# Kernel tuning notes

Hardware: AMD Instinct MI355X
Metric: run time of the kernel (lower is better)

Reference implementation:

```python
import jax, jax.numpy as jnp
import numpy as np

V = 100000
E = 1250000
C_IN = 64
C_OUT = 64


def setup_inputs() -> dict:
    key = jax.random.key(0)
    ks = jax.random.split(key, 6)
    X = jax.random.normal(ks[0], (V, C_IN), dtype=jnp.float32)
    edge_src = jax.random.randint(ks[1], (E,), 0, V, dtype=jnp.int32)
    edge_dst = jax.random.randint(ks[2], (E,), 0, V, dtype=jnp.int32)
    edge_w = jax.random.uniform(ks[3], (E,), dtype=jnp.float32)
    # xavier_normal for (C_IN, C_OUT) weight
    std = float(np.sqrt(2.0 / (C_IN + C_OUT)))
    W = jax.random.normal(ks[4], (C_IN, C_OUT), dtype=jnp.float32) * std
    b = jax.random.normal(ks[5], (C_OUT,), dtype=jnp.float32) * 0.0  # bias init zeros
    return {"X": X, "edge_src": edge_src, "edge_dst": edge_dst,
            "edge_w": edge_w, "W": W, "b": b}


def reference(X, edge_src, edge_dst, edge_w, W, b):
    # f = A @ X  (sparse COO spmm): f[dst] += w * X[src]
    msgs = edge_w[:, None] * X[edge_src]                 # [E, C_IN]
    f = jax.ops.segment_sum(msgs, edge_dst, num_segments=X.shape[0])  # [V, C_IN]
    # out = f @ W + b
    return f @ W + b
```

## Files before the change

kernel.cpp:

```cpp
#include <hip/hip_runtime.h>
#include <hip/hip_fp16.h>


constexpr int V = 100000;
constexpr int E = 1250000;
constexpr int C = 64;

constexpr int NBKT = 1024;
constexpr int VB   = 98;
constexpr int BCAP = 1536;
constexpr int FL   = 8;
constexpr int OVF_CAP = 16384;

constexpr size_t Y_OFF    = 0;
constexpr size_t BIN_OFF  = 12800000;
constexpr size_t GCNT_OFF = 25382912;
constexpr size_t OC_OFF   = 25387008;
constexpr size_t OVF_OFF  = 25387024;
constexpr size_t WS_NEW   = 25649168;

using bf16x8 = __attribute__((ext_vector_type(8))) short;
using f32x4  = __attribute__((ext_vector_type(4))) float;

__device__ __forceinline__ short f2bf(float x) {
    unsigned u = __float_as_uint(x);
    unsigned r = u + 0x7fffu + ((u >> 16) & 1u);
    return (short)(r >> 16);
}
__device__ __forceinline__ float bf2f(short h) {
    return __uint_as_float(((unsigned)(unsigned short)h) << 16);
}

constexpr int ZB  = 1;
constexpr int NBM = 1563;

__global__ __launch_bounds__(256) void zero_xw_kernel(const float* __restrict__ X,
                                                      const float* __restrict__ W,
                                                      __half* __restrict__ Y,
                                                      int* __restrict__ gcnt,
                                                      int* __restrict__ oc) {
    if (blockIdx.x < ZB) {
        int i = threadIdx.x;
        #pragma unroll
        for (int j = 0; j < NBKT / 256; ++j) gcnt[i + j * 256] = 0;
        if (i == 0) *oc = 0;
        return;
    }
    __shared__ short Whi[64 * 72];
    __shared__ short Wlo[64 * 72];
    for (int idx = threadIdx.x; idx < 4096; idx += 256) {
        int k = idx >> 6, c = idx & 63;
        float w  = W[idx];
        short hi = f2bf(w);
        short lo = f2bf(w - bf2f(hi));
        Whi[c * 72 + k] = hi;
        Wlo[c * 72 + k] = lo;
    }
    __syncthreads();

    const int wave = threadIdx.x >> 6;
    const int lane = threadIdx.x & 63;
    const int m = lane & 15;
    const int q = lane >> 4;

    bf16x8 bhi[4][2], blo[4][2];
    #pragma unroll
    for (int t = 0; t < 4; ++t)
        #pragma unroll
        for (int h = 0; h < 2; ++h) {
            int o = (t * 16 + m) * 72 + h * 32 + q * 8;
            bhi[t][h] = *(const bf16x8*)&Whi[o];
            blo[t][h] = *(const bf16x8*)&Wlo[o];
        }

    const int chunk = (blockIdx.x - ZB) * 4 + wave;
    if (chunk >= V / 16) return;
    {
        const float* xp = X + (chunk * 16 + m) * 64 + q * 8;
        bf16x8 ahi[2], alo[2];
        #pragma unroll
        for (int h = 0; h < 2; ++h) {
            float4 f0 = *(const float4*)(xp + h * 32);
            float4 f1 = *(const float4*)(xp + h * 32 + 4);
            float f[8] = {f0.x, f0.y, f0.z, f0.w, f1.x, f1.y, f1.z, f1.w};
            #pragma unroll
            for (int j = 0; j < 8; ++j) {
                short hi = f2bf(f[j]);
                ahi[h][j] = hi;
                alo[h][j] = f2bf(f[j] - bf2f(hi));
            }
        }
        #pragma unroll
        for (int t = 0; t < 4; ++t) {
            f32x4 acc = {0.f, 0.f, 0.f, 0.f};
            #pragma unroll
            for (int h = 0; h < 2; ++h) {
                acc = __builtin_amdgcn_mfma_f32_16x16x32_bf16(ahi[h], bhi[t][h], acc, 0, 0, 0);
                acc = __builtin_amdgcn_mfma_f32_16x16x32_bf16(alo[h], bhi[t][h], acc, 0, 0, 0);
                acc = __builtin_amdgcn_mfma_f32_16x16x32_bf16(ahi[h], blo[t][h], acc, 0, 0, 0);
            }
            #pragma unroll
            for (int i = 0; i < 4; ++i) {
                int row = chunk * 16 + q * 4 + i;
                Y[row * 64 + t * 16 + m] = __float2half(acc[i]);
            }
        }
    }
}

constexpr int BIN_BLOCKS = 512;
constexpr int BIN_T      = 1024;

__global__ __launch_bounds__(BIN_T) void bin_kernel(const int*   __restrict__ esrc,
                                                    const int*   __restrict__ edst,
                                                    const float* __restrict__ ew,
                                                    int*  __restrict__ gcnt,
                                                    int2* __restrict__ binned,
                                                    int*  __restrict__ oc,
                                                    int4* __restrict__ ovf) {
    __shared__ int2 stage[NBKT][FL];
    __shared__ int  lcnt[NBKT];
    for (int i = threadIdx.x; i < NBKT; i += BIN_T) lcnt[i] = 0;
    __syncthreads();

    const int iters = (E + BIN_BLOCKS * BIN_T - 1) / (BIN_BLOCKS * BIN_T);
    for (int it = 0; it < iters; ++it) {
        int e = (it * BIN_BLOCKS + blockIdx.x) * BIN_T + threadIdx.x;
        if (e < E) {
            int d = edst[e];
            int s = esrc[e];
            float w = ew[e];
            int bkt = d / VB;
            int ld  = d - bkt * VB;
            int2 rec = make_int2((ld << 17) | s, __float_as_int(w));
            int pos = atomicAdd(&lcnt[bkt], 1);
            if (pos < FL) {
                stage[bkt][pos] = rec;
            } else {
                int g = atomicAdd(&gcnt[bkt], 1);
                if (g < BCAP) binned[bkt * BCAP + g] = rec;
                else { int p = atomicAdd(oc, 1);
                       if (p < OVF_CAP) ovf[p] = make_int4(s, d, __float_as_int(w), 0); }
            }
        }
    }
    __syncthreads();
    for (int b = threadIdx.x; b < NBKT; b += BIN_T) {
        int n = lcnt[b]; n = n < FL ? n : FL;
        if (n > 0) {
            int g = atomicAdd(&gcnt[b], n);
            for (int i = 0; i < n; ++i) {
                int gi = g + i;
                int2 r = stage[b][i];
                if (gi < BCAP) binned[b * BCAP + gi] = r;
                else { int s = r.x & 0x1FFFF; int ld = r.x >> 17;
                       int p = atomicAdd(oc, 1);
                       if (p < OVF_CAP) ovf[p] = make_int4(s, b * VB + ld, r.y, 0); }
            }
        }
    }
}

__global__ __launch_bounds__(512) void bucket_gather_kernel(const int*  __restrict__ gcnt,
                                                            const int2* __restrict__ binned,
                                                            const int*  __restrict__ oc,
                                                            const int4* __restrict__ ovf,
                                                            const __half* __restrict__ Y,
                                                            const float* __restrict__ bias,
                                                            float* __restrict__ out) {
    __shared__ int2 raw[BCAP];
    __shared__ int2 sorted[BCAP];
    __shared__ int  cnt[VB];
    __shared__ int  pre[VB];
    __shared__ int  cur[VB];
    __shared__ int  buf[128];

    const int tid = threadIdx.x;
    const int b   = blockIdx.x;
    int n = gcnt[b]; n = n < BCAP ? n : BCAP;

    for (int i = tid; i < VB; i += 512) cnt[i] = 0;
    __syncthreads();

    const int2* src = binned + b * BCAP;
    for (int i = tid; i < n; i += 512) {
        int2 r = src[i];
        raw[i] = r;
        atomicAdd(&cnt[r.x >> 17], 1);
    }
    __syncthreads();

    int x = 0;
    if (tid < 128) { x = (tid < VB) ? cnt[tid] : 0; buf[tid] = x; }
    __syncthreads();
    #pragma unroll
    for (int ofs = 1; ofs < 128; ofs <<= 1) {
        int t = 0;
        if (tid < 128 && tid >= ofs) t = buf[tid - ofs];
        __syncthreads();
        if (tid < 128) buf[tid] += t;
        __syncthreads();
    }
    if (tid < VB) { int ex = buf[tid] - x; pre[tid] = ex; cur[tid] = ex; }
    __syncthreads();

    for (int i = tid; i < n; i += 512) {
        int2 r = raw[i];
        int ld = r.x >> 17;
        int p = atomicAdd(&cur[ld], 1);
        sorted[p] = r;
    }
    __syncthreads();

    const int lane = tid & 63;
    const int wv   = tid >> 6;
    float bias_l = bias[lane];
    int ovn = *oc; ovn = ovn < OVF_CAP ? ovn : OVF_CAP;

    for (int ld = wv; ld < VB; ld += 8) {
        int v = b * VB + ld;
        if (v >= V) break;
        int beg = pre[ld];
        int end = beg + cnt[ld];
        float acc = 0.f;
        int i = beg;
        for (; i + 8 <= end; i += 8) {
            int2 r0 = sorted[i],     r1 = sorted[i + 1];
            int2 r2 = sorted[i + 2], r3 = sorted[i + 3];
            int2 r4 = sorted[i + 4], r5 = sorted[i + 5];
            int2 r6 = sorted[i + 6], r7 = sorted[i + 7];
            float y0 = __half2float(Y[(r0.x & 0x1FFFF) * C + lane]);
            float y1 = __half2float(Y[(r1.x & 0x1FFFF) * C + lane]);
            float y2 = __half2float(Y[(r2.x & 0x1FFFF) * C + lane]);
            float y3 = __half2float(Y[(r3.x & 0x1FFFF) * C + lane]);
            float y4 = __half2float(Y[(r4.x & 0x1FFFF) * C + lane]);
            float y5 = __half2float(Y[(r5.x & 0x1FFFF) * C + lane]);
            float y6 = __half2float(Y[(r6.x & 0x1FFFF) * C + lane]);
            float y7 = __half2float(Y[(r7.x & 0x1FFFF) * C + lane]);
            acc += __int_as_float(r0.y) * y0;
            acc += __int_as_float(r1.y) * y1;
            acc += __int_as_float(r2.y) * y2;
            acc += __int_as_float(r3.y) * y3;
            acc += __int_as_float(r4.y) * y4;
            acc += __int_as_float(r5.y) * y5;
            acc += __int_as_float(r6.y) * y6;
            acc += __int_as_float(r7.y) * y7;
        }
        for (; i + 4 <= end; i += 4) {
            int2 r0 = sorted[i], r1 = sorted[i + 1], r2 = sorted[i + 2], r3 = sorted[i + 3];
            float y0 = __half2float(Y[(r0.x & 0x1FFFF) * C + lane]);
            float y1 = __half2float(Y[(r1.x & 0x1FFFF) * C + lane]);
            float y2 = __half2float(Y[(r2.x & 0x1FFFF) * C + lane]);
            float y3 = __half2float(Y[(r3.x & 0x1FFFF) * C + lane]);
            acc += __int_as_float(r0.y) * y0;
            acc += __int_as_float(r1.y) * y1;
            acc += __int_as_float(r2.y) * y2;
            acc += __int_as_float(r3.y) * y3;
        }
        for (; i < end; ++i) {
            int2 rr = sorted[i];
            acc += __int_as_float(rr.y) * __half2float(Y[(rr.x & 0x1FFFF) * C + lane]);
        }
        for (int k = 0; k < ovn; ++k) {
            int4 rr = ovf[k];
            if (rr.y == v)
                acc += __int_as_float(rr.z) * __half2float(Y[rr.x * C + lane]);
        }
        out[v * C + lane] = acc + bias_l;
    }
}

__global__ __launch_bounds__(256) void xw_kernel(const float* __restrict__ X,
                                                 const float* __restrict__ W,
                                                 float* __restrict__ Y) {
    __shared__ float Ws[64][64];
    const float4* W4 = (const float4*)W;
    float4* Ws4 = (float4*)&Ws[0][0];
    #pragma unroll
    for (int i = 0; i < 4; ++i)
        Ws4[threadIdx.x + 256 * i] = W4[threadIdx.x + 256 * i];
    __syncthreads();
    const int wave = threadIdx.x >> 6;
    const int lane = threadIdx.x & 63;
    for (int row = blockIdx.x * 4 + wave; row < V; row += gridDim.x * 4) {
        float xv = X[row * C + lane];
        float acc = 0.f;
        #pragma unroll
        for (int k = 0; k < C; ++k)
            acc += __shfl(xv, k, 64) * Ws[k][lane];
        Y[row * C + lane] = acc;
    }
}

__global__ __launch_bounds__(256) void init_out_kernel(const float* __restrict__ b,
                                                       float4* __restrict__ out4) {
    int tid = blockIdx.x * 256 + threadIdx.x;
    const int n4 = V * (C / 4);
    if (tid < n4) {
        const float4* b4 = (const float4*)b;
        out4[tid] = b4[tid & 15];
    }
}

__global__ __launch_bounds__(256) void scatter_kernel(const int*   __restrict__ esrc,
                                                      const int*   __restrict__ edst,
                                                      const float* __restrict__ ew,
                                                      const float* __restrict__ Y,
                                                      float*       __restrict__ out) {
    unsigned tid = blockIdx.x * 256u + threadIdx.x;
    unsigned e = tid >> 4;
    if (e >= (unsigned)E) return;
    int g = (tid & 15) * 4;
    int   s  = esrc[e];
    int   d  = edst[e];
    float we = ew[e];
    float4 y = *(const float4*)(Y + s * C + g);
    float* o = out + (size_t)d * C + g;
    atomicAdd(o + 0, we * y.x);
    atomicAdd(o + 1, we * y.y);
    atomicAdd(o + 2, we * y.z);
    atomicAdd(o + 3, we * y.w);
}

extern "C" void kernel_launch(void* const* d_in, const int* in_sizes, int n_in,
                              void* d_out, int out_size, void* d_ws, size_t ws_size,
                              hipStream_t stream) {
    const float* X    = (const float*)d_in[0];
    const int*   esrc = (const int*)  d_in[1];
    const int*   edst = (const int*)  d_in[2];
    const float* ew   = (const float*)d_in[3];
    const float* W    = (const float*)d_in[4];
    const float* b    = (const float*)d_in[5];
    float* out = (float*)d_out;

    char* ws = (char*)d_ws;

    if (ws_size >= WS_NEW) {
        __half* Y     = (__half*)(ws + Y_OFF);
        int2*  binned = (int2*)(ws + BIN_OFF);
        int*   gcnt   = (int*) (ws + GCNT_OFF);
        int*   oc     = (int*) (ws + OC_OFF);
        int4*  ovf    = (int4*)(ws + OVF_OFF);

        zero_xw_kernel<<<ZB + NBM, 256, 0, stream>>>(X, W, Y, gcnt, oc);
        bin_kernel<<<BIN_BLOCKS, BIN_T, 0, stream>>>(esrc, edst, ew, gcnt, binned, oc, ovf);
        bucket_gather_kernel<<<NBKT, 512, 0, stream>>>(gcnt, binned, oc, ovf, Y, b, out);
    } else {
        float* Y = (float*)(ws + Y_OFF);
        xw_kernel<<<1024, 256, 0, stream>>>(X, W, Y);
        init_out_kernel<<<(V * (C / 4) + 255) / 256, 256, 0, stream>>>(b, (float4*)out);
        scatter_kernel<<<(E * 16 + 255) / 256, 256, 0, stream>>>(esrc, edst, ew, Y, out);
    }
}
```

Measured before the change: 142.7 us.

## Fuse X·W transform and edge binning into one interleaved kernel launch

Merges the dense X·W MFMA kernel and the edge-binning kernel into a single launch. Blocks are interleaved three XW blocks to two bin blocks, and shared memory is a union of the two stages' buffers. The zeroing of bucket counters moves to a tiny separate kernel. The aim is to overlap the compute-bound GEMM with the atomic-heavy binning and to drop a launch boundary, at the cost of 512-thread bin blocks (down from 1024), more loop iterations, and an extra launch for zeroing.

```diff
diff --git a/kernel.cpp b/kernel.cpp
--- a/kernel.cpp
+++ b/kernel.cpp
@@ -31,131 +31,141 @@
     return __uint_as_float(((unsigned)(unsigned short)h) << 16);
 }
 
-constexpr int ZB  = 1;
-constexpr int NBM = 1563;
-
-__global__ __launch_bounds__(256) void zero_xw_kernel(const float* __restrict__ X,
-                                                      const float* __restrict__ W,
-                                                      __half* __restrict__ Y,
-                                                      int* __restrict__ gcnt,
-                                                      int* __restrict__ oc) {
-    if (blockIdx.x < ZB) {
-        int i = threadIdx.x;
+__global__ __launch_bounds__(256) void zero_kernel(int* __restrict__ gcnt,
+                                                   int* __restrict__ oc) {
+    int i = threadIdx.x;
+    #pragma unroll
+    for (int j = 0; j < NBKT / 256; ++j) gcnt[i + j * 256] = 0;
+    if (i == 0) *oc = 0;
+}
+
+constexpr int FUSE_T    = 512;
+constexpr int XWB       = 782;
+constexpr int BINB      = 512;
+constexpr int FUSE_GRID = 261 * 5;
+
+__global__ __launch_bounds__(FUSE_T) void xwbin_kernel(
+        const float* __restrict__ X,
+        const float* __restrict__ W,
+        __half*      __restrict__ Y,
+        const int*   __restrict__ esrc,
+        const int*   __restrict__ edst,
+        const float* __restrict__ ew,
+        int*  __restrict__ gcnt,
+        int2* __restrict__ binned,
+        int*  __restrict__ oc,
+        int4* __restrict__ ovf) {
+    __shared__ union {
+        struct { short Whi[64 * 72]; short Wlo[64 * 72]; } xw;
+        struct { int2 stage[NBKT][FL]; int lcnt[NBKT]; } bin;
+    } u;
+
+    const int grp  = blockIdx.x / 5;
+    const int slot = blockIdx.x % 5;
+
+    if (slot < 3) {
+        const int xb = grp * 3 + slot;
+        if (xb >= XWB) return;
+
+        for (int idx = threadIdx.x; idx < 4096; idx += FUSE_T) {
+            int k = idx >> 6, c = idx & 63;
+            float w  = W[idx];
+            short hi = f2bf(w);
+            short lo = f2bf(w - bf2f(hi));
+            u.xw.Whi[c * 72 + k] = hi;
+            u.xw.Wlo[c * 72 + k] = lo;
+        }
+        __syncthreads();
+
+        const int wave = threadIdx.x >> 6;
+        const int lane = threadIdx.x & 63;
+        const int m = lane & 15;
+        const int q = lane >> 4;
+
+        bf16x8 bhi[4][2], blo[4][2];
         #pragma unroll
-        for (int j = 0; j < NBKT / 256; ++j) gcnt[i + j * 256] = 0;
-        if (i == 0) *oc = 0;
-        return;
-    }
-    __shared__ short Whi[64 * 72];
-    __shared__ short Wlo[64 * 72];
-    for (int idx = threadIdx.x; idx < 4096; idx += 256) {
-        int k = idx >> 6, c = idx & 63;
-        float w  = W[idx];
-        short hi = f2bf(w);
-        short lo = f2bf(w - bf2f(hi));
-        Whi[c * 72 + k] = hi;
-        Wlo[c * 72 + k] = lo;
-    }
-    __syncthreads();
-
-    const int wave = threadIdx.x >> 6;
-    const int lane = threadIdx.x & 63;
-    const int m = lane & 15;
-    const int q = lane >> 4;
-
-    bf16x8 bhi[4][2], blo[4][2];
-    #pragma unroll
-    for (int t = 0; t < 4; ++t)
-        #pragma unroll
-        for (int h = 0; h < 2; ++h) {
-            int o = (t * 16 + m) * 72 + h * 32 + q * 8;
-            bhi[t][h] = *(const bf16x8*)&Whi[o];
-            blo[t][h] = *(const bf16x8*)&Wlo[o];
-        }
-
-    const int chunk = (blockIdx.x - ZB) * 4 + wave;
-    if (chunk >= V / 16) return;
-    {
-        const float* xp = X + (chunk * 16 + m) * 64 + q * 8;
-        bf16x8 ahi[2], alo[2];
-        #pragma unroll
-        for (int h = 0; h < 2; ++h) {
-            float4 f0 = *(const float4*)(xp + h * 32);
-            float4 f1 = *(const float4*)(xp + h * 32 + 4);
-            float f[8] = {f0.x, f0.y, f0.z, f0.w, f1.x, f1.y, f1.z, f1.w};
-            #pragma unroll
-            for (int j = 0; j < 8; ++j) {
-                short hi = f2bf(f[j]);
-                ahi[h][j] = hi;
-                alo[h][j] = f2bf(f[j] - bf2f(hi));
-            }
-        }
-        #pragma unroll
-        for (int t = 0; t < 4; ++t) {
-            f32x4 acc = {0.f, 0.f, 0.f, 0.f};
+        for (int t = 0; t < 4; ++t)
             #pragma unroll
             for (int h = 0; h < 2; ++h) {
-                acc = __builtin_amdgcn_mfma_f32_16x16x32_bf16(ahi[h], bhi[t][h], acc, 0, 0, 0);
-                acc = __builtin_amdgcn_mfma_f32_16x16x32_bf16(alo[h], bhi[t][h], acc, 0, 0, 0);
-                acc = __builtin_amdgcn_mfma_f32_16x16x32_bf16(ahi[h], blo[t][h], acc, 0, 0, 0);
-            }
+                int o = (t * 16 + m) * 72 + h * 32 + q * 8;
+                bhi[t][h] = *(const bf16x8*)&u.xw.Whi[o];
+                blo[t][h] = *(const bf16x8*)&u.xw.Wlo[o];
+            }
+
+        const int chunk = xb * 8 + wave;
+        if (chunk >= V / 16) return;
+        {
+            const float* xp = X + (chunk * 16 + m) * 64 + q * 8;
+            bf16x8 ahi[2], alo[2];
             #pragma unroll
-            for (int i = 0; i < 4; ++i) {
-                int row = chunk * 16 + q * 4 + i;
-                Y[row * 64 + t * 16 + m] = __float2half(acc[i]);
-            }
-        }
-    }
-}
-
-constexpr int BIN_BLOCKS = 512;
-constexpr int BIN_T      = 1024;
-
-__global__ __launch_bounds__(BIN_T) void bin_kernel(const int*   __restrict__ esrc,
-                                                    const int*   __restrict__ edst,
-                                                    const float* __restrict__ ew,
-                                                    int*  __restrict__ gcnt,
-                                                    int2* __restrict__ binned,
-                                                    int*  __restrict__ oc,
-                                                    int4* __restrict__ ovf) {
-    __shared__ int2 stage[NBKT][FL];
-    __shared__ int  lcnt[NBKT];
-    for (int i = threadIdx.x; i < NBKT; i += BIN_T) lcnt[i] = 0;
-    __syncthreads();
-
-    const int iters = (E + BIN_BLOCKS * BIN_T - 1) / (BIN_BLOCKS * BIN_T);
-    for (int it = 0; it < iters; ++it) {
-        int e = (it * BIN_BLOCKS + blockIdx.x) * BIN_T + threadIdx.x;
-        if (e < E) {
-            int d = edst[e];
-            int s = esrc[e];
-            float w = ew[e];
-            int bkt = d / VB;
-            int ld  = d - bkt * VB;
-            int2 rec = make_int2((ld << 17) | s, __float_as_int(w));
-            int pos = atomicAdd(&lcnt[bkt], 1);
-            if (pos < FL) {
-                stage[bkt][pos] = rec;
-            } else {
-                int g = atomicAdd(&gcnt[bkt], 1);
-                if (g < BCAP) binned[bkt * BCAP + g] = rec;
-                else { int p = atomicAdd(oc, 1);
-                       if (p < OVF_CAP) ovf[p] = make_int4(s, d, __float_as_int(w), 0); }
-            }
-        }
-    }
-    __syncthreads();
-    for (int b = threadIdx.x; b < NBKT; b += BIN_T) {
-        int n = lcnt[b]; n = n < FL ? n : FL;
-        if (n > 0) {
-            int g = atomicAdd(&gcnt[b], n);
-            for (int i = 0; i < n; ++i) {
-                int gi = g + i;
-                int2 r = stage[b][i];
-                if (gi < BCAP) binned[b * BCAP + gi] = r;
-                else { int s = r.x & 0x1FFFF; int ld = r.x >> 17;
-                       int p = atomicAdd(oc, 1);
-                       if (p < OVF_CAP) ovf[p] = make_int4(s, b * VB + ld, r.y, 0); }
+            for (int h = 0; h < 2; ++h) {
+                float4 f0 = *(const float4*)(xp + h * 32);
+                float4 f1 = *(const float4*)(xp + h * 32 + 4);
+                float f[8] = {f0.x, f0.y, f0.z, f0.w, f1.x, f1.y, f1.z, f1.w};
+                #pragma unroll
+                for (int j = 0; j < 8; ++j) {
+                    short hi = f2bf(f[j]);
+                    ahi[h][j] = hi;
+                    alo[h][j] = f2bf(f[j] - bf2f(hi));
+                }
+            }
+            #pragma unroll
+            for (int t = 0; t < 4; ++t) {
+                f32x4 acc = {0.f, 0.f, 0.f, 0.f};
+                #pragma unroll
+                for (int h = 0; h < 2; ++h) {
+                    acc = __builtin_amdgcn_mfma_f32_16x16x32_bf16(ahi[h], bhi[t][h], acc, 0, 0, 0);
+                    acc = __builtin_amdgcn_mfma_f32_16x16x32_bf16(alo[h], bhi[t][h], acc, 0, 0, 0);
+                    acc = __builtin_amdgcn_mfma_f32_16x16x32_bf16(ahi[h], blo[t][h], acc, 0, 0, 0);
+                }
+                #pragma unroll
+                for (int i = 0; i < 4; ++i) {
+                    int row = chunk * 16 + q * 4 + i;
+                    Y[row * 64 + t * 16 + m] = __float2half(acc[i]);
+                }
+            }
+        }
+    } else {
+        const int bb = grp * 2 + (slot - 3);
+        if (bb >= BINB) return;
+
+        for (int i = threadIdx.x; i < NBKT; i += FUSE_T) u.bin.lcnt[i] = 0;
+        __syncthreads();
+
+        const int iters = (E + BINB * FUSE_T - 1) / (BINB * FUSE_T);
+        for (int it = 0; it < iters; ++it) {
+            int e = (it * BINB + bb) * FUSE_T + threadIdx.x;
+            if (e < E) {
+                int d = edst[e];
+                int s = esrc[e];
+                float w = ew[e];
+                int bkt = d / VB;
+                int ld  = d - bkt * VB;
+                int2 rec = make_int2((ld << 17) | s, __float_as_int(w));
+                int pos = atomicAdd(&u.bin.lcnt[bkt], 1);
+                if (pos < FL) {
+                    u.bin.stage[bkt][pos] = rec;
+                } else {
+                    int g = atomicAdd(&gcnt[bkt], 1);
+                    if (g < BCAP) binned[bkt * BCAP + g] = rec;
+                    else { int p = atomicAdd(oc, 1);
+                           if (p < OVF_CAP) ovf[p] = make_int4(s, d, __float_as_int(w), 0); }
+                }
+            }
+        }
+        __syncthreads();
+        for (int b = threadIdx.x; b < NBKT; b += FUSE_T) {
+            int n = u.bin.lcnt[b]; n = n < FL ? n : FL;
+            if (n > 0) {
+                int g = atomicAdd(&gcnt[b], n);
+                for (int i = 0; i < n; ++i) {
+                    int gi = g + i;
+                    int2 r = u.bin.stage[b][i];
+                    if (gi < BCAP) binned[b * BCAP + gi] = r;
+                    else { int s = r.x & 0x1FFFF; int ld = r.x >> 17;
+                           int p = atomicAdd(oc, 1);
+                           if (p < OVF_CAP) ovf[p] = make_int4(s, b * VB + ld, r.y, 0); }
+                }
             }
         }
     }
@@ -342,8 +352,9 @@
         int*   oc     = (int*) (ws + OC_OFF);
         int4*  ovf    = (int4*)(ws + OVF_OFF);
 
-        zero_xw_kernel<<<ZB + NBM, 256, 0, stream>>>(X, W, Y, gcnt, oc);
-        bin_kernel<<<BIN_BLOCKS, BIN_T, 0, stream>>>(esrc, edst, ew, gcnt, binned, oc, ovf);
+        zero_kernel<<<1, 256, 0, stream>>>(gcnt, oc);
+        xwbin_kernel<<<FUSE_GRID, FUSE_T, 0, stream>>>(X, W, Y, esrc, edst, ew,
+                                                       gcnt, binned, oc, ovf);
         bucket_gather_kernel<<<NBKT, 512, 0, stream>>>(gcnt, binned, oc, ovf, Y, b, out);
     } else {
         float* Y = (float*)(ws + Y_OFF);
```

New measurement: 140.0 us (median of 2 runs). No clear change (-1.9%).
